# Kernel optimization log

Hardware: AMD Instinct MI355X
Metric: run time of the kernel (lower is better)

Reference implementation:

```python
import jax, jax.numpy as jnp
import numpy as np

N_NODES = 262144
N_EDGES = 2097152
N_GRAPHS = 8192
IN_CH = 54
HID = 32
OUT_CH = 64
SLOPE = 0.01  # AttentiveFP uses leaky_relu / GATConv negative_slope=0.01
NUM_TIMESTEPS = 2


def _gru(x, h, wih, whh, bih, bhh):
    # torch.nn.GRUCell semantics
    gi = x @ wih.T + bih
    gh = h @ whh.T + bhh
    ir, iz, inn = jnp.split(gi, 3, axis=-1)
    hr, hz, hn = jnp.split(gh, 3, axis=-1)
    r = jax.nn.sigmoid(ir + hr)
    z = jax.nn.sigmoid(iz + hz)
    n = jnp.tanh(inn + r * hn)
    return (1.0 - z) * n + z * h


def _seg_softmax(a, idx, n):
    # PyG softmax over edges grouped by target index
    m = jax.ops.segment_max(a, idx, num_segments=n)
    e = jnp.exp(a - m[idx])
    s = jax.ops.segment_sum(e, idx, num_segments=n)
    return e / (s[idx] + 1e-16)


def _forward(x, edge_attr,
             lin1_w, lin1_b,
             g_lin1_w, g_lin2_w, g_att_l, g_att_r, g_bias,
             gru1_wih, gru1_whh, gru1_bih, gru1_bhh,
             a_lin_w, a_att_src, a_att_dst, a_bias,
             gru2_wih, gru2_whh, gru2_bih, gru2_bhh,
             m_lin_w, m_att_src, m_att_dst, m_bias,
             gru3_wih, gru3_whh, gru3_bih, gru3_bhh,
             lin2_w, lin2_b,
             edge_index, batch_index):
    src, dst = edge_index[0], edge_index[1]  # j -> i (source_to_target)
    n = x.shape[0]
    # Atom embedding
    x = jax.nn.leaky_relu(x @ lin1_w.T + lin1_b, SLOPE)
    # --- GATEConv (first layer, uses edge features) ---
    xj, xi = x[src], x[dst]
    e = jax.nn.leaky_relu(jnp.concatenate([xj, edge_attr], axis=-1) @ g_lin1_w.T, SLOPE)
    alpha = jax.nn.leaky_relu(e @ g_att_l + xi @ g_att_r, SLOPE)
    alpha = _seg_softmax(alpha, dst, n)
    h = jax.ops.segment_sum((xj @ g_lin2_w.T) * alpha[:, None], dst, num_segments=n) + g_bias
    h = jax.nn.elu(h)
    x = jax.nn.relu(_gru(h, x, gru1_wih, gru1_whh, gru1_bih, gru1_bhh))
    # --- GATConv atom layer (num_layers=2 -> one extra conv) ---
    xt = x @ a_lin_w.T
    al = xt @ a_att_src
    ar = xt @ a_att_dst
    alpha = jax.nn.leaky_relu(al[src] + ar[dst], SLOPE)
    alpha = _seg_softmax(alpha, dst, n)
    h = jax.ops.segment_sum(xt[src] * alpha[:, None], dst, num_segments=n) + a_bias
    h = jax.nn.elu(h)
    x = jax.nn.relu(_gru(h, x, gru2_wih, gru2_whh, gru2_bih, gru2_bhh))
    # --- Molecule readout: iterative GAT attention from nodes to their graph ---
    out = jax.nn.relu(jax.ops.segment_sum(x, batch_index, num_segments=N_GRAPHS))
    xs = x @ m_lin_w.T          # transformed node (source) features, fixed per step
    a_node = xs @ m_att_src     # per-node attention logit contribution
    for _ in range(NUM_TIMESTEPS):
        a_g = (out @ m_lin_w.T) @ m_att_dst  # per-graph contribution
        alpha = jax.nn.leaky_relu(a_node + a_g[batch_index], SLOPE)
        alpha = _seg_softmax(alpha, batch_index, N_GRAPHS)
        h = jax.ops.segment_sum(xs * alpha[:, None], batch_index, num_segments=N_GRAPHS) + m_bias
        h = jax.nn.elu(h)
        out = jax.nn.relu(_gru(h, out, gru3_wih, gru3_whh, gru3_bih, gru3_bhh))
    out = out @ lin2_w.T + lin2_b
    # Mish activation wrapper
    return out * jnp.tanh(jax.nn.softplus(out))


def setup_inputs() -> dict:
    key = jax.random.key(0)
    ks = jax.random.split(key, 24)
    def rn(k, shape, s=0.1):
        return jax.random.normal(k, shape, dtype=jnp.float32) * s
    z = lambda *s: jnp.zeros(s, jnp.float32)
    return {
        "x": jax.random.normal(ks[0], (N_NODES, IN_CH), dtype=jnp.float32),
        "edge_attr": jax.random.normal(ks[1], (N_EDGES, 1), dtype=jnp.float32),
        "edge_index": jax.random.randint(ks[2], (2, N_EDGES), 0, N_NODES, dtype=jnp.int32),
        "batch_index": jnp.sort(jax.random.randint(ks[3], (N_NODES,), 0, N_GRAPHS, dtype=jnp.int32)),
        "lin1_w": rn(ks[4], (HID, IN_CH)), "lin1_b": z(HID),
        "g_lin1_w": rn(ks[5], (HID, HID + 1)),
        "g_lin2_w": rn(ks[6], (HID, HID)),
        "g_att_l": rn(ks[7], (HID,)), "g_att_r": rn(ks[8], (HID,)),
        "g_bias": z(HID),
        "gru1_wih": rn(ks[9], (3 * HID, HID)), "gru1_whh": rn(ks[10], (3 * HID, HID)),
        "gru1_bih": z(3 * HID), "gru1_bhh": z(3 * HID),
        "a_lin_w": rn(ks[11], (HID, HID)),
        "a_att_src": rn(ks[12], (HID,)), "a_att_dst": rn(ks[13], (HID,)),
        "a_bias": z(HID),
        "gru2_wih": rn(ks[14], (3 * HID, HID)), "gru2_whh": rn(ks[15], (3 * HID, HID)),
        "gru2_bih": z(3 * HID), "gru2_bhh": z(3 * HID),
        "m_lin_w": rn(ks[16], (HID, HID)),
        "m_att_src": rn(ks[17], (HID,)), "m_att_dst": rn(ks[18], (HID,)),
        "m_bias": z(HID),
        "gru3_wih": rn(ks[19], (3 * HID, HID)), "gru3_whh": rn(ks[20], (3 * HID, HID)),
        "gru3_bih": z(3 * HID), "gru3_bhh": z(3 * HID),
        "lin2_w": rn(ks[21], (OUT_CH, HID)), "lin2_b": z(OUT_CH),
    }


def reference(x, edge_attr, edge_index, batch_index,
              lin1_w, lin1_b,
              g_lin1_w, g_lin2_w, g_att_l, g_att_r, g_bias,
              gru1_wih, gru1_whh, gru1_bih, gru1_bhh,
              a_lin_w, a_att_src, a_att_dst, a_bias,
              gru2_wih, gru2_whh, gru2_bih, gru2_bhh,
              m_lin_w, m_att_src, m_att_dst, m_bias,
              gru3_wih, gru3_whh, gru3_bih, gru3_bhh,
              lin2_w, lin2_b):
    return _forward(x, edge_attr,
                    lin1_w, lin1_b,
                    g_lin1_w, g_lin2_w, g_att_l, g_att_r, g_bias,
                    gru1_wih, gru1_whh, gru1_bih, gru1_bhh,
                    a_lin_w, a_att_src, a_att_dst, a_bias,
                    gru2_wih, gru2_whh, gru2_bih, gru2_bhh,
                    m_lin_w, m_att_src, m_att_dst, m_bias,
                    gru3_wih, gru3_whh, gru3_bih, gru3_bhh,
                    lin2_w, lin2_b,
                    edge_index, batch_index)
```

## Files before the change

kernel.cpp:

```cpp
#include <hip/hip_runtime.h>
#include <hip/hip_bf16.h>
#include <math.h>

#define NN 262144
#define NE 2097152
#define NG 8192
#define THREADS 256

typedef __hip_bfloat16 bf16;
typedef __attribute__((ext_vector_type(8))) short short8v;
typedef __attribute__((ext_vector_type(4))) float f32x4;

static __device__ __forceinline__ float lrelu(float x){ return x > 0.f ? x : 0.01f*x; }
static __device__ __forceinline__ float eluf(float x){ return x > 0.f ? x : __expf(x) - 1.f; }
static __device__ __forceinline__ float sigm(float x){ return 1.f/(1.f + __expf(-x)); }
static __device__ __forceinline__ float tanh_fast(float x){
  float e = __expf(2.f*x); return 1.f - 2.f/(e + 1.f);
}
static __device__ __forceinline__ float b2f(bf16 v){ return __bfloat162float(v); }
static __device__ __forceinline__ bf16 f2b(float v){ return __float2bfloat16(v); }
static __device__ __forceinline__ float s2f(short s){
  return __uint_as_float(((unsigned int)(unsigned short)s) << 16);
}

static __device__ __forceinline__ unsigned short bfbits(float f){
  union { bf16 b; unsigned short s; } u; u.b = f2b(f); return u.s;
}
static __device__ __forceinline__ unsigned int pack2(float lo, float hi){
  return (unsigned int)bfbits(lo) | ((unsigned int)bfbits(hi) << 16);
}

static __device__ __forceinline__ float redsum32(float t){
  #pragma unroll
  for (int o = 16; o > 0; o >>= 1) t += __shfl_xor(t, o, 32);
  return t;
}

static __device__ __forceinline__ float gru_relu(float hv, float xv, int c,
    const float* __restrict__ wih, const float* __restrict__ whh,
    const float* __restrict__ bih, const float* __restrict__ bhh){
  float gr = bih[c], gz = bih[32+c], gn = bih[64+c];
  float hr = bhh[c], hz = bhh[32+c], hn = bhh[64+c];
  #pragma unroll 8
  for (int k = 0; k < 32; k++){
    float hk = __shfl(hv, k, 32);
    float xk = __shfl(xv, k, 32);
    gr += hk*wih[(     c)*32 + k];
    gz += hk*wih[(32 + c)*32 + k];
    gn += hk*wih[(64 + c)*32 + k];
    hr += xk*whh[(     c)*32 + k];
    hz += xk*whh[(32 + c)*32 + k];
    hn += xk*whh[(64 + c)*32 + k];
  }
  float r = sigm(gr + hr), z = sigm(gz + hz);
  float nn2 = tanh_fast(gn + r*hn);
  return fmaxf((1.f - z)*nn2 + z*xv, 0.f);
}

__global__ __launch_bounds__(THREADS) void k_filli(int* __restrict__ p, int v, int n){
  int i = blockIdx.x*THREADS + threadIdx.x;
  if (i < n) p[i] = v;
}

#define FB_EMBED 512
#define FB_HIST  8192
#define FB_GPTR  1024

__global__ __launch_bounds__(THREADS) void k_front(
    const float* __restrict__ xin, const float* __restrict__ lw, const float* __restrict__ lb,
    const float* __restrict__ w1, const float* __restrict__ w2,
    const float* __restrict__ attr_r, float* __restrict__ X,
    bf16* __restrict__ u, bf16* __restrict__ v, float* __restrict__ nr,
    const int* __restrict__ ei, int* __restrict__ hist, int* __restrict__ rank,
    const int* __restrict__ batch, int* __restrict__ gptr){
  __shared__ float ol[4][16][33];
  int bid = blockIdx.x;
  if (bid < FB_EMBED){
    int wid  = bid*4 + (threadIdx.x >> 6);
    int wv   = threadIdx.x >> 6;
    int lane = threadIdx.x & 63;
    int cl = lane & 15;
    int kb = lane >> 4;
    short8v BL[2][2], BU[2], BV[2];
    #pragma unroll
    for (int g = 0; g < 2; g++){
      #pragma unroll
      for (int kc = 0; kc < 2; kc++){
        short8v t;
        #pragma unroll
        for (int j = 0; j < 8; j++){
          int k = kc*32 + kb*8 + j;
          t[j] = (k < 54) ? (short)bfbits(lw[(size_t)(g*16+cl)*54 + k]) : (short)0;
        }
        BL[g][kc] = t;
      }
      short8v tu, tv;
      #pragma unroll
      for (int j = 0; j < 8; j++){
        tu[j] = (short)bfbits(w1[(size_t)(g*16+cl)*33 + kb*8 + j]);
        tv[j] = (short)bfbits(w2[(size_t)(g*16+cl)*32 + kb*8 + j]);
      }
      BU[g] = tu; BV[g] = tv;
    }
    float bb0 = lb[cl], bb1 = lb[16+cl];
    float ar0 = attr_r[cl], ar1 = attr_r[16+cl];
    f32x4 zero; zero[0]=0.f; zero[1]=0.f; zero[2]=0.f; zero[3]=0.f;

    for (int t = 0; t < 8; t++){
      int nb = (wid*8 + t)*16;
      const float* xrow = xin + (size_t)(nb + cl)*54;
      short8v Ax0, Ax1;
      const float2* x2 = (const float2*)(xrow + kb*8);
      #pragma unroll
      for (int jj = 0; jj < 4; jj++){
        float2 tvv = x2[jj];
        Ax0[2*jj]   = (short)bfbits(tvv.x);
        Ax0[2*jj+1] = (short)bfbits(tvv.y);
      }
      #pragma unroll
      for (int j = 0; j < 8; j++){
        int k = 32 + kb*8 + j;
        Ax1[j] = (k < 54) ? (short)bfbits(xrow[k]) : (short)0;
      }
      f32x4 a0, a1;
      #pragma unroll
      for (int q = 0; q < 4; q++){ a0[q] = bb0; a1[q] = bb1; }
      f32x4 d0 = __builtin_amdgcn_mfma_f32_16x16x32_bf16(Ax0, BL[0][0], a0, 0, 0, 0);
      d0 = __builtin_amdgcn_mfma_f32_16x16x32_bf16(Ax1, BL[0][1], d0, 0, 0, 0);
      f32x4 d1 = __builtin_amdgcn_mfma_f32_16x16x32_bf16(Ax0, BL[1][0], a1, 0, 0, 0);
      d1 = __builtin_amdgcn_mfma_f32_16x16x32_bf16(Ax1, BL[1][1], d1, 0, 0, 0);
      #pragma unroll
      for (int r = 0; r < 4; r++){ d0[r] = lrelu(d0[r]); d1[r] = lrelu(d1[r]); }
      #pragma unroll
      for (int r = 0; r < 4; r++){
        int node = nb + kb*4 + r;
        float* srow = X + (size_t)node*32;
        srow[cl]      = d0[r];
        srow[16 + cl] = d1[r];
        ol[wv][kb*4 + r][cl]      = d0[r];
        ol[wv][kb*4 + r][16 + cl] = d1[r];
      }
      #pragma unroll
      for (int r = 0; r < 4; r++){
        float vsum = d0[r]*ar0 + d1[r]*ar1;
        vsum += __shfl_xor(vsum, 1, 16);
        vsum += __shfl_xor(vsum, 2, 16);
        vsum += __shfl_xor(vsum, 4, 16);
        vsum += __shfl_xor(vsum, 8, 16);
        if (cl == 0) nr[nb + kb*4 + r] = vsum;
      }
      __syncthreads();
      short8v Ao;
      #pragma unroll
      for (int j = 0; j < 8; j++) Ao[j] = (short)bfbits(ol[wv][cl][kb*8 + j]);
      f32x4 u0 = __builtin_amdgcn_mfma_f32_16x16x32_bf16(Ao, BU[0], zero, 0, 0, 0);
      f32x4 u1 = __builtin_amdgcn_mfma_f32_16x16x32_bf16(Ao, BU[1], zero, 0, 0, 0);
      f32x4 v0 = __builtin_amdgcn_mfma_f32_16x16x32_bf16(Ao, BV[0], zero, 0, 0, 0);
      f32x4 v1 = __builtin_amdgcn_mfma_f32_16x16x32_bf16(Ao, BV[1], zero, 0, 0, 0);
      #pragma unroll
      for (int r = 0; r < 4; r++){
        int node = nb + kb*4 + r;
        bf16* ur = u + (size_t)node*32;
        bf16* vr = v + (size_t)node*32;
        ur[cl]      = f2b(u0[r]);
        ur[16 + cl] = f2b(u1[r]);
        vr[cl]      = f2b(v0[r]);
        vr[16 + cl] = f2b(v1[r]);
      }
      __syncthreads();
    }
  } else if (bid < FB_EMBED + FB_HIST){
    int e = (bid - FB_EMBED)*THREADS + threadIdx.x;
    rank[e] = atomicAdd(hist + ei[NE + e], 1);
  } else {
    int n = (bid - FB_EMBED - FB_HIST)*THREADS + threadIdx.x;
    int bc = batch[n];
    if (n == 0){ for (int g = 0; g <= bc; g++) gptr[g] = 0; }
    else {
      int pb = batch[n-1];
      if (pb != bc) for (int g = pb+1; g <= bc; g++) gptr[g] = n;
    }
    if (n == NN-1){ for (int g = bc+1; g <= NG; g++) gptr[g] = NN; }
  }
}

__global__ __launch_bounds__(THREADS) void k_scan1(const int* __restrict__ hist,
    int* __restrict__ rp1, int* __restrict__ btot){
  __shared__ int sh[THREADS];
  int i = blockIdx.x*THREADS + threadIdx.x;
  int v = hist[i];
  sh[threadIdx.x] = v; __syncthreads();
  #pragma unroll
  for (int off = 1; off < THREADS; off <<= 1){
    int t = (threadIdx.x >= off) ? sh[threadIdx.x - off] : 0;
    __syncthreads(); sh[threadIdx.x] += t; __syncthreads();
  }
  rp1[i] = sh[threadIdx.x] - v;
  if (threadIdx.x == THREADS-1) btot[blockIdx.x] = sh[THREADS-1];
}

__global__ __launch_bounds__(1024) void k_scan2(int* __restrict__ btot){
  __shared__ int sh[1024];
  int i = threadIdx.x;
  int v = btot[i];
  sh[i] = v; __syncthreads();
  for (int off = 1; off < 1024; off <<= 1){
    int t = (i >= off) ? sh[i - off] : 0;
    __syncthreads(); sh[i] += t; __syncthreads();
  }
  btot[i] = sh[i] - v;
}

#define MB_SCAN 1024

__global__ __launch_bounds__(THREADS) void k_mid(const int* __restrict__ rp1,
    const int* __restrict__ btot, int* __restrict__ rowptr,
    const int* __restrict__ ei, const float* __restrict__ ea,
    const int* __restrict__ rank, int2* __restrict__ epk){
  int bid = blockIdx.x;
  if (bid < MB_SCAN){
    int i = bid*THREADS + threadIdx.x;
    rowptr[i] = rp1[i] + btot[i >> 8];
    if (i == 0) rowptr[NN] = NE;
  } else {
    int e = (bid - MB_SCAN)*THREADS + threadIdx.x;
    int d = ei[NE + e];
    int pos = rp1[d] + btot[d >> 8] + rank[e];
    epk[pos] = make_int2(ei[e], __float_as_int(ea[e]));
  }
}

__global__ __launch_bounds__(THREADS) void k_gru_att(const bf16* __restrict__ HV,
    float* __restrict__ S,
    const float* __restrict__ wih, const float* __restrict__ whh,
    const float* __restrict__ bih, const float* __restrict__ bhh,
    const float* __restrict__ attW, const float* __restrict__ att1,
    const float* __restrict__ att2,
    bf16* __restrict__ xt, float* __restrict__ s1, float* __restrict__ s2){
  __shared__ float ol[4][16][33];
  int wid  = (blockIdx.x*THREADS + threadIdx.x) >> 6;
  int wv   = threadIdx.x >> 6;
  int lane = threadIdx.x & 63;
  int cl = lane & 15;
  int kb = lane >> 4;
  short8v BW[12], BT[2];
  #pragma unroll
  for (int g = 0; g < 6; g++){
    const float* wr = wih + (size_t)(g*16 + cl)*32 + kb*8;
    const float* vr = whh + (size_t)(g*16 + cl)*32 + kb*8;
    short8v bw, bv;
    #pragma unroll
    for (int j = 0; j < 8; j++){ bw[j] = (short)bfbits(wr[j]); bv[j] = (short)bfbits(vr[j]); }
    BW[g] = bw; BW[6+g] = bv;
  }
  #pragma unroll
  for (int g = 0; g < 2; g++){
    short8v bt;
    #pragma unroll
    for (int j = 0; j < 8; j++) bt[j] = (short)bfbits(attW[(size_t)(g*16+cl)*32 + kb*8 + j]);
    BT[g] = bt;
  }
  float bI[6], bH[6];
  #pragma unroll
  for (int g = 0; g < 6; g++){ bI[g] = bih[g*16 + cl]; bH[g] = bhh[g*16 + cl]; }
  float a1c0 = att1[cl], a1c1 = att1[16+cl];
  float a2c0 = att2 ? att2[cl] : 0.f, a2c1 = att2 ? att2[16+cl] : 0.f;
  f32x4 zero; zero[0]=0.f; zero[1]=0.f; zero[2]=0.f; zero[3]=0.f;

  for (int t = 0; t < 8; t++){
    int nb = (wid*8 + t) * 16;
    short8v Ah = *(const short8v*)(HV + (size_t)(nb + cl)*32 + kb*8);
    const float* xr = S + (size_t)(nb + cl)*32 + kb*8;
    short8v Ax;
    #pragma unroll
    for (int j = 0; j < 8; j++) Ax[j] = (short)bfbits(xr[j]);
    f32x4 gi[6], gh[6];
    #pragma unroll
    for (int g = 0; g < 6; g++){
      f32x4 a, b;
      #pragma unroll
      for (int q = 0; q < 4; q++){ a[q] = bI[g]; b[q] = bH[g]; }
      gi[g] = __builtin_amdgcn_mfma_f32_16x16x32_bf16(Ah, BW[g],   a, 0, 0, 0);
      gh[g] = __builtin_amdgcn_mfma_f32_16x16x32_bf16(Ax, BW[6+g], b, 0, 0, 0);
    }
    #pragma unroll
    for (int r = 0; r < 4; r++){
      int node = nb + kb*4 + r;
      float* srow = S + (size_t)node*32;
      float x0 = srow[cl], x1 = srow[16 + cl];
      float r0 = sigm(gi[0][r] + gh[0][r]);
      float z0 = sigm(gi[2][r] + gh[2][r]);
      float n0 = tanh_fast(gi[4][r] + r0*gh[4][r]);
      float r1 = sigm(gi[1][r] + gh[1][r]);
      float z1 = sigm(gi[3][r] + gh[3][r]);
      float n1 = tanh_fast(gi[5][r] + r1*gh[5][r]);
      float o0 = fmaxf((1.f - z0)*n0 + z0*x0, 0.f);
      float o1 = fmaxf((1.f - z1)*n1 + z1*x1, 0.f);
      srow[cl]      = o0;
      srow[16 + cl] = o1;
      ol[wv][kb*4 + r][cl]      = o0;
      ol[wv][kb*4 + r][16 + cl] = o1;
    }
    __syncthreads();
    short8v Ao;
    #pragma unroll
    for (int j = 0; j < 8; j++) Ao[j] = (short)bfbits(ol[wv][cl][kb*8 + j]);
    f32x4 t0 = __builtin_amdgcn_mfma_f32_16x16x32_bf16(Ao, BT[0], zero, 0, 0, 0);
    f32x4 t1 = __builtin_amdgcn_mfma_f32_16x16x32_bf16(Ao, BT[1], zero, 0, 0, 0);
    #pragma unroll
    for (int r = 0; r < 4; r++){
      int node = nb + kb*4 + r;
      bf16* xrow = xt + (size_t)node*32;
      xrow[cl]      = f2b(t0[r]);
      xrow[16 + cl] = f2b(t1[r]);
      float p1 = t0[r]*a1c0 + t1[r]*a1c1;
      p1 += __shfl_xor(p1, 1, 16);
      p1 += __shfl_xor(p1, 2, 16);
      p1 += __shfl_xor(p1, 4, 16);
      p1 += __shfl_xor(p1, 8, 16);
      if (cl == 0) s1[node] = p1;
      if (att2){
        float p2 = t0[r]*a2c0 + t1[r]*a2c1;
        p2 += __shfl_xor(p2, 1, 16);
        p2 += __shfl_xor(p2, 2, 16);
        p2 += __shfl_xor(p2, 4, 16);
        p2 += __shfl_xor(p2, 8, 16);
        if (cl == 0) s2[node] = p2;
      }
    }
    __syncthreads();
  }
}

__global__ __launch_bounds__(THREADS) void k_conv(const int* __restrict__ rowptr,
    const int2* __restrict__ epk, const bf16* __restrict__ U,
    const float* __restrict__ w1 , const float* __restrict__ attl,
    const float* __restrict__ alsrc, const float* __restrict__ term,
    const bf16* __restrict__ ROWS, const float* __restrict__ bias,
    bf16* __restrict__ HV){
  int node = blockIdx.x*(THREADS/32) + (threadIdx.x >> 5);
  int c32 = threadIdx.x & 31;
  int ws = rowptr[node], we = rowptr[node+1];
  float tv = term[node];
  float wc[32], at[32];
  if (U){
    #pragma unroll
    for (int j = 0; j < 32; j++){ wc[j] = w1[j*33 + 32]; at[j] = attl[j]; }
  }
  int eg = c32 >> 2, cb = c32 & 3;
  float s = 0.f;
  float acc[8];
  #pragma unroll
  for (int j = 0; j < 8; j++) acc[j] = 0.f;
  for (int p0 = ws; p0 < we; p0 += 32){
    int p = p0 + c32;
    bool ok = p < we;
    int pc = ok ? p : ws;
    int2 pk = epk[pc];
    int siA = pk.x;
    float sc;
    if (U){
      float a = __int_as_float(pk.y);
      const short8v* ur = (const short8v*)(U + (size_t)siA*32);
      sc = 0.f;
      #pragma unroll
      for (int q = 0; q < 4; q++){
        short8v u8 = ur[q];
        #pragma unroll
        for (int j = 0; j < 8; j++)
          sc += at[q*8+j]*lrelu(s2f(u8[j]) + a*wc[q*8+j]);
      }
    } else {
      sc = alsrc[siA];
    }
    float wme = ok ? __expf(lrelu(sc + tv)) : 0.f;
    s += redsum32(wme);
    #pragma unroll
    for (int s8 = 0; s8 < 32; s8 += 8){
      if (p0 + s8 >= we) break;
      float w = __shfl(wme, s8 + eg, 32);
      int si  = __shfl(siA, s8 + eg, 32);
      short8v r8 = *(const short8v*)(ROWS + (size_t)si*32 + cb*8);
      #pragma unroll
      for (int j = 0; j < 8; j++) acc[j] += s2f(r8[j]) * w;
    }
  }
  float inv = 1.f/(s + 1e-16f);
  #pragma unroll
  for (int j = 0; j < 8; j++){
    acc[j] += __shfl_xor(acc[j], 4, 32);
    acc[j] += __shfl_xor(acc[j], 8, 32);
    acc[j] += __shfl_xor(acc[j], 16, 32);
  }
  if (eg == 0){
    unsigned int o[4];
    #pragma unroll
    for (int j2 = 0; j2 < 4; j2++){
      float h0 = eluf(acc[2*j2  ]*inv + bias[cb*8 + 2*j2  ]);
      float h1 = eluf(acc[2*j2+1]*inv + bias[cb*8 + 2*j2+1]);
      o[j2] = pack2(h0, h1);
    }
    *(uint4*)(HV + (size_t)node*32 + cb*8) = make_uint4(o[0], o[1], o[2], o[3]);
  }
}

#define TB_RSUM 1024

__global__ __launch_bounds__(THREADS) void k_tail(const int* __restrict__ gptr,
    const float* __restrict__ X, float* __restrict__ gout,
    const float* __restrict__ mw, const float* __restrict__ mattd,
    float* __restrict__ q){
  int bid = blockIdx.x;
  if (bid < TB_RSUM){
    int g = bid*(THREADS/32) + (threadIdx.x >> 5);
    int c = threadIdx.x & 31;
    int gs = gptr[g], ge = gptr[g+1];
    float acc = 0.f;
    for (int n = gs; n < ge; n++) acc += X[(size_t)n*32 + c];
    gout[(size_t)g*32 + c] = fmaxf(acc, 0.f);
  } else {
    int k = threadIdx.x;
    if (k < 32){
      float acc = 0.f;
      #pragma unroll
      for (int c = 0; c < 32; c++) acc += mattd[c] * mw[c*32 + k];
      q[k] = acc;
    }
  }
}

__global__ __launch_bounds__(THREADS) void k_rstep(const int* __restrict__ gptr,
    const float* __restrict__ anode, const bf16* __restrict__ XS,
    const float* __restrict__ q, const float* __restrict__ mbias,
    float* __restrict__ gout,
    const float* __restrict__ wih, const float* __restrict__ whh,
    const float* __restrict__ bih, const float* __restrict__ bhh){
  int g = blockIdx.x*(THREADS/32) + (threadIdx.x >> 5);
  int c = threadIdx.x & 31;
  float orow = gout[(size_t)g*32 + c];
  float ag = redsum32(orow * q[c]);
  int gs = gptr[g], ge = gptr[g+1];
  float s = 0.f;
  for (int p0 = gs; p0 < ge; p0 += 32){
    int p = p0 + c;
    bool ok = p < ge;
    float e = ok ? __expf(lrelu(anode[p] + ag)) : 0.f;
    s += redsum32(e);
  }
  float inv = 1.f/(s + 1e-16f);
  float acc = 0.f;
  int n = gs;
  for (; n + 4 <= ge; n += 4){
    float e0 = __expf(lrelu(anode[n]   + ag));
    float e1 = __expf(lrelu(anode[n+1] + ag));
    float e2 = __expf(lrelu(anode[n+2] + ag));
    float e3 = __expf(lrelu(anode[n+3] + ag));
    acc += b2f(XS[(size_t)(n  )*32 + c])*e0 + b2f(XS[(size_t)(n+1)*32 + c])*e1
         + b2f(XS[(size_t)(n+2)*32 + c])*e2 + b2f(XS[(size_t)(n+3)*32 + c])*e3;
  }
  for (; n < ge; n++)
    acc += b2f(XS[(size_t)n*32 + c]) * __expf(lrelu(anode[n] + ag));
  acc *= inv;
  float hv = eluf(acc + mbias[c]);
  gout[(size_t)g*32 + c] = gru_relu(hv, orow, c, wih, whh, bih, bhh);
}

__global__ __launch_bounds__(THREADS) void k_final(const float* __restrict__ out32,
    const float* __restrict__ w , const float* __restrict__ b,
    float* __restrict__ y){
  int gid = blockIdx.x*THREADS + threadIdx.x;
  int g = gid >> 6, oc = gid & 63;
  const float* orow = out32 + (size_t)g*32;
  const float* wr = w + oc*32;
  float acc = b[oc];
  #pragma unroll
  for (int k = 0; k < 32; k++) acc += orow[k]*wr[k];
  float sp = fmaxf(acc, 0.f) + log1pf(expf(-fabsf(acc)));
  y[(size_t)g*64 + oc] = acc * tanhf(sp);
}

extern "C" void kernel_launch(void* const* d_in, const int* in_sizes, int n_in,
                              void* d_out, int out_size, void* d_ws, size_t ws_size,
                              hipStream_t stream){
  const float* x_in     = (const float*)d_in[0];
  const float* ea       = (const float*)d_in[1];
  const int*   ei       = (const int*)  d_in[2];
  const int*   batch    = (const int*)  d_in[3];
  const float* lin1_w   = (const float*)d_in[4];
  const float* lin1_b   = (const float*)d_in[5];
  const float* g_lin1_w = (const float*)d_in[6];
  const float* g_lin2_w = (const float*)d_in[7];
  const float* g_att_l  = (const float*)d_in[8];
  const float* g_att_r  = (const float*)d_in[9];
  const float* g_bias   = (const float*)d_in[10];
  const float* gru1_wih = (const float*)d_in[11];
  const float* gru1_whh = (const float*)d_in[12];
  const float* gru1_bih = (const float*)d_in[13];
  const float* gru1_bhh = (const float*)d_in[14];
  const float* a_lin_w  = (const float*)d_in[15];
  const float* a_att_src= (const float*)d_in[16];
  const float* a_att_dst= (const float*)d_in[17];
  const float* a_bias   = (const float*)d_in[18];
  const float* gru2_wih = (const float*)d_in[19];
  const float* gru2_whh = (const float*)d_in[20];
  const float* gru2_bih = (const float*)d_in[21];
  const float* gru2_bhh = (const float*)d_in[22];
  const float* m_lin_w  = (const float*)d_in[23];
  const float* m_att_src= (const float*)d_in[24];
  const float* m_att_dst= (const float*)d_in[25];
  const float* m_bias   = (const float*)d_in[26];
  const float* gru3_wih = (const float*)d_in[27];
  const float* gru3_whh = (const float*)d_in[28];
  const float* gru3_bih = (const float*)d_in[29];
  const float* gru3_bhh = (const float*)d_in[30];
  const float* lin2_w   = (const float*)d_in[31];
  const float* lin2_b   = (const float*)d_in[32];

  float* W = (float*)d_ws;
  float* X     = W;
  bf16*  BA    = (bf16*)(W + 8388608);
  bf16*  BB    = (bf16*)(W + 12582912);
  int2*  EPK   = (int2*) (W + 16777216);
  int*   RP1   = (int*)  (W + 20971520);
  bf16*  BC    = (bf16*) (W + 20971520);
  int*   RANK  = (int*)  (W + 23068672);
  int*   ROWPTR= (int*)  (W + 25165824);
  int*   HIST  = (int*)  (W + 25428032);
  int*   BTOT  = (int*)  (W + 25690176);
  float* NS1   = W + 25691200;
  float* NS2   = W + 25953344;
  int*   GPTR  = (int*)  (W + 26215488);
  float* GOUT  = W + 26223744;
  float* Q     = W + 26485888;

  dim3 b(THREADS);
  const int gNode  = NN/THREADS;
  const int gNode32= NN/(THREADS/32);
  const int gG32   = NG/(THREADS/32);
  const int gMFMA  = NN/(16*8*4);

  k_filli<<<gNode, b, 0, stream>>>(HIST, 0, NN);

  k_front<<<FB_EMBED + FB_HIST + FB_GPTR, b, 0, stream>>>(
      x_in, lin1_w, lin1_b, g_lin1_w, g_lin2_w, g_att_r, X, BA, BB, NS1,
      ei, HIST, RANK, batch, GPTR);

  k_scan1<<<gNode, b, 0, stream>>>(HIST, RP1, BTOT);
  k_scan2<<<1, 1024, 0, stream>>>(BTOT);
  k_mid<<<MB_SCAN + NE/THREADS, b, 0, stream>>>(RP1, BTOT, ROWPTR, ei, ea, RANK, EPK);

  k_conv<<<gNode32, b, 0, stream>>>(ROWPTR, EPK, BA, g_lin1_w, g_att_l,
      nullptr, NS1, BB, g_bias, BC);
  k_gru_att<<<gMFMA, b, 0, stream>>>(BC, X, gru1_wih, gru1_whh, gru1_bih, gru1_bhh,
      a_lin_w, a_att_src, a_att_dst, BA, NS1, NS2);

  k_conv<<<gNode32, b, 0, stream>>>(ROWPTR, EPK, nullptr, nullptr, nullptr,
      NS1, NS2, BA, a_bias, BB);
  k_gru_att<<<gMFMA, b, 0, stream>>>(BB, X, gru2_wih, gru2_whh, gru2_bih, gru2_bhh,
      m_lin_w, m_att_src, nullptr, BA, NS1, nullptr);

  k_tail<<<TB_RSUM + 1, b, 0, stream>>>(GPTR, X, GOUT, m_lin_w, m_att_dst, Q);

  for (int t = 0; t < 2; t++){
    k_rstep<<<gG32, b, 0, stream>>>(GPTR, NS1, BA, Q, m_bias, GOUT,
        gru3_wih, gru3_whh, gru3_bih, gru3_bhh);
  }

  k_final<<<(NG*64)/THREADS, b, 0, stream>>>(GOUT, lin2_w, lin2_b, (float*)d_out);
}
```

Measured before the change: 469.8 us.

## Fuse conv aggregation with GRU/attention, and fuse readout steps with final linear

Merges each edge-softmax aggregation kernel with the following GRU+attention-projection kernel. The aggregated hidden rows stay in shared memory instead of being written to and re-read from global bf16 buffers. The three readout-stage kernels (sum pooling, two attention/GRU steps, final linear+mish) are also combined into one per-graph kernel. This removes launches and intermediate global traffic. In exchange, each block now does 64 nodes' conv work with 8 nodes per 32-lane group serially before the MFMA stage, which may reduce parallelism and latency hiding for the gather phase.

```diff
diff --git a/kernel.cpp b/kernel.cpp
--- a/kernel.cpp
+++ b/kernel.cpp
@@ -230,46 +230,118 @@
   }
 }
 
-__global__ __launch_bounds__(THREADS) void k_gru_att(const bf16* __restrict__ HV,
+__global__ __launch_bounds__(THREADS) void k_conv_gru(const int* __restrict__ rowptr,
+    const int2* __restrict__ epk, const bf16* __restrict__ U,
+    const float* __restrict__ w1 , const float* __restrict__ attl,
+    const float* __restrict__ alsrc, const float* __restrict__ term,
+    const bf16* __restrict__ ROWS, const float* __restrict__ bias,
     float* __restrict__ S,
     const float* __restrict__ wih, const float* __restrict__ whh,
     const float* __restrict__ bih, const float* __restrict__ bhh,
     const float* __restrict__ attW, const float* __restrict__ att1,
     const float* __restrict__ att2,
     bf16* __restrict__ xt, float* __restrict__ s1, float* __restrict__ s2){
-  __shared__ float ol[4][16][33];
-  int wid  = (blockIdx.x*THREADS + threadIdx.x) >> 6;
-  int wv   = threadIdx.x >> 6;
-  int lane = threadIdx.x & 63;
-  int cl = lane & 15;
-  int kb = lane >> 4;
-  short8v BW[12], BT[2];
-  #pragma unroll
-  for (int g = 0; g < 6; g++){
-    const float* wr = wih + (size_t)(g*16 + cl)*32 + kb*8;
-    const float* vr = whh + (size_t)(g*16 + cl)*32 + kb*8;
-    short8v bw, bv;
-    #pragma unroll
-    for (int j = 0; j < 8; j++){ bw[j] = (short)bfbits(wr[j]); bv[j] = (short)bfbits(vr[j]); }
-    BW[g] = bw; BW[6+g] = bv;
-  }
-  #pragma unroll
-  for (int g = 0; g < 2; g++){
-    short8v bt;
-    #pragma unroll
-    for (int j = 0; j < 8; j++) bt[j] = (short)bfbits(attW[(size_t)(g*16+cl)*32 + kb*8 + j]);
-    BT[g] = bt;
-  }
-  float bI[6], bH[6];
-  #pragma unroll
-  for (int g = 0; g < 6; g++){ bI[g] = bih[g*16 + cl]; bH[g] = bhh[g*16 + cl]; }
-  float a1c0 = att1[cl], a1c1 = att1[16+cl];
-  float a2c0 = att2 ? att2[cl] : 0.f, a2c1 = att2 ? att2[16+cl] : 0.f;
-  f32x4 zero; zero[0]=0.f; zero[1]=0.f; zero[2]=0.f; zero[3]=0.f;
-
-  for (int t = 0; t < 8; t++){
-    int nb = (wid*8 + t) * 16;
-    short8v Ah = *(const short8v*)(HV + (size_t)(nb + cl)*32 + kb*8);
+  __shared__ float hl[64][33];
+  int nb0 = (int)blockIdx.x * 64;
+  {
+    int g = threadIdx.x >> 5;
+    int c32 = threadIdx.x & 31;
+    float wc[32], at[32];
+    if (U){
+      #pragma unroll
+      for (int j = 0; j < 32; j++){ wc[j] = w1[j*33 + 32]; at[j] = attl[j]; }
+    }
+    int eg = c32 >> 2, cb = c32 & 3;
+    for (int i = 0; i < 8; i++){
+      int ln = g*8 + i;
+      int node = nb0 + ln;
+      int ws = rowptr[node], we = rowptr[node+1];
+      float tv = term[node];
+      float s = 0.f;
+      float acc[8];
+      #pragma unroll
+      for (int j = 0; j < 8; j++) acc[j] = 0.f;
+      for (int p0 = ws; p0 < we; p0 += 32){
+        int p = p0 + c32;
+        bool ok = p < we;
+        int pc = ok ? p : ws;
+        int2 pk = epk[pc];
+        int siA = pk.x;
+        float sc;
+        if (U){
+          float a = __int_as_float(pk.y);
+          const short8v* ur = (const short8v*)(U + (size_t)siA*32);
+          sc = 0.f;
+          #pragma unroll
+          for (int q = 0; q < 4; q++){
+            short8v u8 = ur[q];
+            #pragma unroll
+            for (int j = 0; j < 8; j++)
+              sc += at[q*8+j]*lrelu(s2f(u8[j]) + a*wc[q*8+j]);
+          }
+        } else {
+          sc = alsrc[siA];
+        }
+        float wme = ok ? __expf(lrelu(sc + tv)) : 0.f;
+        s += redsum32(wme);
+        #pragma unroll
+        for (int s8 = 0; s8 < 32; s8 += 8){
+          if (p0 + s8 >= we) break;
+          float w = __shfl(wme, s8 + eg, 32);
+          int si  = __shfl(siA, s8 + eg, 32);
+          short8v r8 = *(const short8v*)(ROWS + (size_t)si*32 + cb*8);
+          #pragma unroll
+          for (int j = 0; j < 8; j++) acc[j] += s2f(r8[j]) * w;
+        }
+      }
+      float inv = 1.f/(s + 1e-16f);
+      #pragma unroll
+      for (int j = 0; j < 8; j++){
+        acc[j] += __shfl_xor(acc[j], 4, 32);
+        acc[j] += __shfl_xor(acc[j], 8, 32);
+        acc[j] += __shfl_xor(acc[j], 16, 32);
+      }
+      if (eg == 0){
+        #pragma unroll
+        for (int j = 0; j < 8; j++)
+          hl[ln][cb*8 + j] = eluf(acc[j]*inv + bias[cb*8 + j]);
+      }
+    }
+  }
+  __syncthreads();
+  {
+    int wv   = threadIdx.x >> 6;
+    int lane = threadIdx.x & 63;
+    int cl = lane & 15;
+    int kb = lane >> 4;
+    short8v BW[12], BT[2];
+    #pragma unroll
+    for (int g = 0; g < 6; g++){
+      const float* wr = wih + (size_t)(g*16 + cl)*32 + kb*8;
+      const float* vr = whh + (size_t)(g*16 + cl)*32 + kb*8;
+      short8v bw, bv;
+      #pragma unroll
+      for (int j = 0; j < 8; j++){ bw[j] = (short)bfbits(wr[j]); bv[j] = (short)bfbits(vr[j]); }
+      BW[g] = bw; BW[6+g] = bv;
+    }
+    #pragma unroll
+    for (int g = 0; g < 2; g++){
+      short8v bt;
+      #pragma unroll
+      for (int j = 0; j < 8; j++) bt[j] = (short)bfbits(attW[(size_t)(g*16+cl)*32 + kb*8 + j]);
+      BT[g] = bt;
+    }
+    float bI[6], bH[6];
+    #pragma unroll
+    for (int g = 0; g < 6; g++){ bI[g] = bih[g*16 + cl]; bH[g] = bhh[g*16 + cl]; }
+    float a1c0 = att1[cl], a1c1 = att1[16+cl];
+    float a2c0 = att2 ? att2[cl] : 0.f, a2c1 = att2 ? att2[16+cl] : 0.f;
+    f32x4 zero; zero[0]=0.f; zero[1]=0.f; zero[2]=0.f; zero[3]=0.f;
+
+    int nb = nb0 + wv*16;
+    short8v Ah;
+    #pragma unroll
+    for (int j = 0; j < 8; j++) Ah[j] = (short)bfbits(hl[wv*16 + cl][kb*8 + j]);
     const float* xr = S + (size_t)(nb + cl)*32 + kb*8;
     short8v Ax;
     #pragma unroll
@@ -298,13 +370,12 @@
       float o1 = fmaxf((1.f - z1)*n1 + z1*x1, 0.f);
       srow[cl]      = o0;
       srow[16 + cl] = o1;
-      ol[wv][kb*4 + r][cl]      = o0;
-      ol[wv][kb*4 + r][16 + cl] = o1;
-    }
-    __syncthreads();
+      hl[wv*16 + kb*4 + r][cl]      = o0;
+      hl[wv*16 + kb*4 + r][16 + cl] = o1;
+    }
     short8v Ao;
     #pragma unroll
-    for (int j = 0; j < 8; j++) Ao[j] = (short)bfbits(ol[wv][cl][kb*8 + j]);
+    for (int j = 0; j < 8; j++) Ao[j] = (short)bfbits(hl[wv*16 + cl][kb*8 + j]);
     f32x4 t0 = __builtin_amdgcn_mfma_f32_16x16x32_bf16(Ao, BT[0], zero, 0, 0, 0);
     f32x4 t1 = __builtin_amdgcn_mfma_f32_16x16x32_bf16(Ao, BT[1], zero, 0, 0, 0);
     #pragma unroll
@@ -328,155 +399,63 @@
         if (cl == 0) s2[node] = p2;
       }
     }
-    __syncthreads();
-  }
-}
-
-__global__ __launch_bounds__(THREADS) void k_conv(const int* __restrict__ rowptr,
-    const int2* __restrict__ epk, const bf16* __restrict__ U,
-    const float* __restrict__ w1 , const float* __restrict__ attl,
-    const float* __restrict__ alsrc, const float* __restrict__ term,
-    const bf16* __restrict__ ROWS, const float* __restrict__ bias,
-    bf16* __restrict__ HV){
-  int node = blockIdx.x*(THREADS/32) + (threadIdx.x >> 5);
-  int c32 = threadIdx.x & 31;
-  int ws = rowptr[node], we = rowptr[node+1];
-  float tv = term[node];
-  float wc[32], at[32];
-  if (U){
-    #pragma unroll
-    for (int j = 0; j < 32; j++){ wc[j] = w1[j*33 + 32]; at[j] = attl[j]; }
-  }
-  int eg = c32 >> 2, cb = c32 & 3;
-  float s = 0.f;
-  float acc[8];
-  #pragma unroll
-  for (int j = 0; j < 8; j++) acc[j] = 0.f;
-  for (int p0 = ws; p0 < we; p0 += 32){
-    int p = p0 + c32;
-    bool ok = p < we;
-    int pc = ok ? p : ws;
-    int2 pk = epk[pc];
-    int siA = pk.x;
-    float sc;
-    if (U){
-      float a = __int_as_float(pk.y);
-      const short8v* ur = (const short8v*)(U + (size_t)siA*32);
-      sc = 0.f;
-      #pragma unroll
-      for (int q = 0; q < 4; q++){
-        short8v u8 = ur[q];
-        #pragma unroll
-        for (int j = 0; j < 8; j++)
-          sc += at[q*8+j]*lrelu(s2f(u8[j]) + a*wc[q*8+j]);
-      }
-    } else {
-      sc = alsrc[siA];
-    }
-    float wme = ok ? __expf(lrelu(sc + tv)) : 0.f;
-    s += redsum32(wme);
-    #pragma unroll
-    for (int s8 = 0; s8 < 32; s8 += 8){
-      if (p0 + s8 >= we) break;
-      float w = __shfl(wme, s8 + eg, 32);
-      int si  = __shfl(siA, s8 + eg, 32);
-      short8v r8 = *(const short8v*)(ROWS + (size_t)si*32 + cb*8);
-      #pragma unroll
-      for (int j = 0; j < 8; j++) acc[j] += s2f(r8[j]) * w;
-    }
-  }
-  float inv = 1.f/(s + 1e-16f);
-  #pragma unroll
-  for (int j = 0; j < 8; j++){
-    acc[j] += __shfl_xor(acc[j], 4, 32);
-    acc[j] += __shfl_xor(acc[j], 8, 32);
-    acc[j] += __shfl_xor(acc[j], 16, 32);
-  }
-  if (eg == 0){
-    unsigned int o[4];
-    #pragma unroll
-    for (int j2 = 0; j2 < 4; j2++){
-      float h0 = eluf(acc[2*j2  ]*inv + bias[cb*8 + 2*j2  ]);
-      float h1 = eluf(acc[2*j2+1]*inv + bias[cb*8 + 2*j2+1]);
-      o[j2] = pack2(h0, h1);
-    }
-    *(uint4*)(HV + (size_t)node*32 + cb*8) = make_uint4(o[0], o[1], o[2], o[3]);
-  }
-}
-
-#define TB_RSUM 1024
-
-__global__ __launch_bounds__(THREADS) void k_tail(const int* __restrict__ gptr,
-    const float* __restrict__ X, float* __restrict__ gout,
-    const float* __restrict__ mw, const float* __restrict__ mattd,
-    float* __restrict__ q){
-  int bid = blockIdx.x;
-  if (bid < TB_RSUM){
-    int g = bid*(THREADS/32) + (threadIdx.x >> 5);
-    int c = threadIdx.x & 31;
-    int gs = gptr[g], ge = gptr[g+1];
-    float acc = 0.f;
-    for (int n = gs; n < ge; n++) acc += X[(size_t)n*32 + c];
-    gout[(size_t)g*32 + c] = fmaxf(acc, 0.f);
-  } else {
-    int k = threadIdx.x;
-    if (k < 32){
-      float acc = 0.f;
-      #pragma unroll
-      for (int c = 0; c < 32; c++) acc += mattd[c] * mw[c*32 + k];
-      q[k] = acc;
-    }
-  }
-}
-
-__global__ __launch_bounds__(THREADS) void k_rstep(const int* __restrict__ gptr,
-    const float* __restrict__ anode, const bf16* __restrict__ XS,
-    const float* __restrict__ q, const float* __restrict__ mbias,
-    float* __restrict__ gout,
+  }
+}
+
+__global__ __launch_bounds__(THREADS) void k_readout(const int* __restrict__ gptr,
+    const float* __restrict__ X, const float* __restrict__ anode,
+    const bf16* __restrict__ XS,
+    const float* __restrict__ mw , const float* __restrict__ mattd,
+    const float* __restrict__ mbias,
     const float* __restrict__ wih, const float* __restrict__ whh,
-    const float* __restrict__ bih, const float* __restrict__ bhh){
+    const float* __restrict__ bih, const float* __restrict__ bhh,
+    const float* __restrict__ lin2_w, const float* __restrict__ lin2_b,
+    float* __restrict__ y){
   int g = blockIdx.x*(THREADS/32) + (threadIdx.x >> 5);
   int c = threadIdx.x & 31;
-  float orow = gout[(size_t)g*32 + c];
-  float ag = redsum32(orow * q[c]);
   int gs = gptr[g], ge = gptr[g+1];
-  float s = 0.f;
-  for (int p0 = gs; p0 < ge; p0 += 32){
-    int p = p0 + c;
-    bool ok = p < ge;
-    float e = ok ? __expf(lrelu(anode[p] + ag)) : 0.f;
-    s += redsum32(e);
-  }
-  float inv = 1.f/(s + 1e-16f);
-  float acc = 0.f;
-  int n = gs;
-  for (; n + 4 <= ge; n += 4){
-    float e0 = __expf(lrelu(anode[n]   + ag));
-    float e1 = __expf(lrelu(anode[n+1] + ag));
-    float e2 = __expf(lrelu(anode[n+2] + ag));
-    float e3 = __expf(lrelu(anode[n+3] + ag));
-    acc += b2f(XS[(size_t)(n  )*32 + c])*e0 + b2f(XS[(size_t)(n+1)*32 + c])*e1
-         + b2f(XS[(size_t)(n+2)*32 + c])*e2 + b2f(XS[(size_t)(n+3)*32 + c])*e3;
-  }
-  for (; n < ge; n++)
-    acc += b2f(XS[(size_t)n*32 + c]) * __expf(lrelu(anode[n] + ag));
-  acc *= inv;
-  float hv = eluf(acc + mbias[c]);
-  gout[(size_t)g*32 + c] = gru_relu(hv, orow, c, wih, whh, bih, bhh);
-}
-
-__global__ __launch_bounds__(THREADS) void k_final(const float* __restrict__ out32,
-    const float* __restrict__ w , const float* __restrict__ b,
-    float* __restrict__ y){
-  int gid = blockIdx.x*THREADS + threadIdx.x;
-  int g = gid >> 6, oc = gid & 63;
-  const float* orow = out32 + (size_t)g*32;
-  const float* wr = w + oc*32;
-  float acc = b[oc];
+  float out = 0.f;
+  for (int n = gs; n < ge; n++) out += X[(size_t)n*32 + c];
+  out = fmaxf(out, 0.f);
+  float qc = 0.f;
   #pragma unroll
-  for (int k = 0; k < 32; k++) acc += orow[k]*wr[k];
-  float sp = fmaxf(acc, 0.f) + log1pf(expf(-fabsf(acc)));
-  y[(size_t)g*64 + oc] = acc * tanhf(sp);
+  for (int j = 0; j < 32; j++) qc += mattd[j]*mw[j*32 + c];
+  #pragma unroll 1
+  for (int t = 0; t < 2; t++){
+    float ag = redsum32(out * qc);
+    float s = 0.f;
+    for (int p0 = gs; p0 < ge; p0 += 32){
+      int p = p0 + c;
+      float e = (p < ge) ? __expf(lrelu(anode[p] + ag)) : 0.f;
+      s += redsum32(e);
+    }
+    float inv = 1.f/(s + 1e-16f);
+    float acc = 0.f;
+    int n = gs;
+    for (; n + 4 <= ge; n += 4){
+      float e0 = __expf(lrelu(anode[n]   + ag));
+      float e1 = __expf(lrelu(anode[n+1] + ag));
+      float e2 = __expf(lrelu(anode[n+2] + ag));
+      float e3 = __expf(lrelu(anode[n+3] + ag));
+      acc += b2f(XS[(size_t)(n  )*32 + c])*e0 + b2f(XS[(size_t)(n+1)*32 + c])*e1
+           + b2f(XS[(size_t)(n+2)*32 + c])*e2 + b2f(XS[(size_t)(n+3)*32 + c])*e3;
+    }
+    for (; n < ge; n++)
+      acc += b2f(XS[(size_t)n*32 + c]) * __expf(lrelu(anode[n] + ag));
+    acc *= inv;
+    float hv = eluf(acc + mbias[c]);
+    out = gru_relu(hv, out, c, wih, whh, bih, bhh);
+  }
+  #pragma unroll
+  for (int oc2 = 0; oc2 < 2; oc2++){
+    int oc = oc2*32 + c;
+    float facc = lin2_b[oc];
+    const float* wr = lin2_w + (size_t)oc*32;
+    #pragma unroll 8
+    for (int k = 0; k < 32; k++) facc += __shfl(out, k, 32) * wr[k];
+    float sp = fmaxf(facc, 0.f) + log1pf(expf(-fabsf(facc)));
+    y[(size_t)g*64 + oc] = facc * tanhf(sp);
+  }
 }
 
 extern "C" void kernel_launch(void* const* d_in, const int* in_sizes, int n_in,
@@ -530,14 +509,13 @@
   float* NS1   = W + 25691200;
   float* NS2   = W + 25953344;
   int*   GPTR  = (int*)  (W + 26215488);
-  float* GOUT  = W + 26223744;
-  float* Q     = W + 26485888;
+  float* NS3   = W + 26223744;
+  float* NS4   = W + 26485888;
 
   dim3 b(THREADS);
   const int gNode  = NN/THREADS;
-  const int gNode32= NN/(THREADS/32);
-  const int gG32   = NG/(THREADS/32);
-  const int gMFMA  = NN/(16*8*4);
+  const int gCG    = NN/64;
+  const int gRO    = NG/(THREADS/32);
 
   k_filli<<<gNode, b, 0, stream>>>(HIST, 0, NN);
 
@@ -549,22 +527,16 @@
   k_scan2<<<1, 1024, 0, stream>>>(BTOT);
   k_mid<<<MB_SCAN + NE/THREADS, b, 0, stream>>>(RP1, BTOT, ROWPTR, ei, ea, RANK, EPK);
 
-  k_conv<<<gNode32, b, 0, stream>>>(ROWPTR, EPK, BA, g_lin1_w, g_att_l,
-      nullptr, NS1, BB, g_bias, BC);
-  k_gru_att<<<gMFMA, b, 0, stream>>>(BC, X, gru1_wih, gru1_whh, gru1_bih, gru1_bhh,
-      a_lin_w, a_att_src, a_att_dst, BA, NS1, NS2);
-
-  k_conv<<<gNode32, b, 0, stream>>>(ROWPTR, EPK, nullptr, nullptr, nullptr,
-      NS1, NS2, BA, a_bias, BB);
-  k_gru_att<<<gMFMA, b, 0, stream>>>(BB, X, gru2_wih, gru2_whh, gru2_bih, gru2_bhh,
+  k_conv_gru<<<gCG, b, 0, stream>>>(ROWPTR, EPK, BA, g_lin1_w, g_att_l,
+      nullptr, NS1, BB, g_bias, X,
+      gru1_wih, gru1_whh, gru1_bih, gru1_bhh,
+      a_lin_w, a_att_src, a_att_dst, BC, NS3, NS4);
+
+  k_conv_gru<<<gCG, b, 0, stream>>>(ROWPTR, EPK, nullptr, nullptr, nullptr,
+      NS3, NS4, BC, a_bias, X,
+      gru2_wih, gru2_whh, gru2_bih, gru2_bhh,
       m_lin_w, m_att_src, nullptr, BA, NS1, nullptr);
 
-  k_tail<<<TB_RSUM + 1, b, 0, stream>>>(GPTR, X, GOUT, m_lin_w, m_att_dst, Q);
-
-  for (int t = 0; t < 2; t++){
-    k_rstep<<<gG32, b, 0, stream>>>(GPTR, NS1, BA, Q, m_bias, GOUT,
-        gru3_wih, gru3_whh, gru3_bih, gru3_bhh);
-  }
-
-  k_final<<<(NG*64)/THREADS, b, 0, stream>>>(GOUT, lin2_w, lin2_b, (float*)d_out);
-}
+  k_readout<<<gRO, b, 0, stream>>>(GPTR, X, NS1, BA, m_lin_w, m_att_dst, m_bias,
+      gru3_wih, gru3_whh, gru3_bih, gru3_bhh, lin2_w, lin2_b, (float*)d_out);
+}
```

After: 598.7 us. 1.27x slower.
